# Kernel optimization log

Hardware: AMD Instinct MI355X
Metric: run time of the kernel (lower is better)

Reference implementation:

```python
import jax, jax.numpy as jnp
import numpy as np

D_MODEL = 1024
N_EXPERTS = 8
HIDDEN = 2048
TOP_K = 2


def setup_inputs() -> dict:
    key = jax.random.key(0)
    ks = jax.random.split(key, 5)
    scale_in = 1.0 / np.sqrt(D_MODEL)
    scale_h = 1.0 / np.sqrt(HIDDEN)
    return {
        "x": jax.random.normal(ks[0], (2, 2048, D_MODEL), dtype=jnp.float32),
        "w_router": jax.random.normal(ks[1], (D_MODEL, N_EXPERTS), dtype=jnp.float32) * scale_in,
        "w1": jax.random.normal(ks[2], (N_EXPERTS, D_MODEL, HIDDEN), dtype=jnp.float32) * scale_in,
        "w3": jax.random.normal(ks[3], (N_EXPERTS, D_MODEL, HIDDEN), dtype=jnp.float32) * scale_in,
        "w2": jax.random.normal(ks[4], (N_EXPERTS, HIDDEN, D_MODEL), dtype=jnp.float32) * scale_h,
    }


def reference(x, w_router, w1, w3, w2):
    orig_shape = x.shape
    xt = x.reshape(-1, orig_shape[-1])            # [T, D]
    T = xt.shape[0]

    # Router: linear -> softmax -> top-k (weights = top-k softmax scores)
    logits = xt @ w_router                         # [T, E]
    scores = jax.nn.softmax(logits, axis=-1)       # [T, E]
    top_w, top_idx = jax.lax.top_k(scores, TOP_K)  # [T, K]

    # Dense routing-weight matrix (reference form of dispatch/combine)
    dense_w = jnp.zeros((T, N_EXPERTS), dtype=scores.dtype)
    dense_w = dense_w.at[jnp.arange(T)[:, None], top_idx].set(top_w)  # [T, E]

    # Per-expert SwiGLU MLP over all tokens (dense reference of grouped GEMM)
    h1 = jnp.einsum('td,edh->teh', xt, w1)         # [T, E, H]
    h3 = jnp.einsum('td,edh->teh', xt, w3)
    h = jax.nn.silu(h1) * h3                       # [T, E, H]
    y = jnp.einsum('teh,ehd->ted', h, w2)          # [T, E, D]

    # Combine with routing weights
    out = jnp.einsum('te,ted->td', dense_w, y)     # [T, D]
    return out.reshape(orig_shape)
```

## Files before the change

kernel.cpp:

```cpp
#include <hip/hip_runtime.h>
#include <stdint.h>

#define D_MODEL 1024
#define N_EXP   8
#define HIDDEN  2048
#define TOPK    2

#define BK    32
#define PADM  128
#define NT1   (D_MODEL / BK)
#define NT2   (HIDDEN / BK)
#define G1X   1152
#define G2X   288

typedef short bf16x8 __attribute__((ext_vector_type(8)));
typedef float f32x4 __attribute__((ext_vector_type(4)));
typedef unsigned u32x4 __attribute__((ext_vector_type(4)));

__device__ __forceinline__ unsigned short f2bf(float f) {
    union { float f; unsigned u; } v; v.f = f;
    unsigned r = v.u + 0x7fffu + ((v.u >> 16) & 1u);
    return (unsigned short)(r >> 16);
}

__device__ __forceinline__ float bf2f(unsigned short u) {
    union { unsigned u; float f; } v; v.u = (unsigned)u << 16; return v.f;
}

__device__ __forceinline__ void gload_lds16(const void* g, void* l) {
    __builtin_amdgcn_global_load_lds(
        (const __attribute__((address_space(1))) void*)g,
        (__attribute__((address_space(3))) void*)l, 16, 0, 0);
}

__global__ __launch_bounds__(256) void k_prep(
    const float* __restrict__ x, const float* __restrict__ wr,
    const float* __restrict__ w1, const float* __restrict__ w3, const float* __restrict__ w2,
    unsigned short* __restrict__ xb,
    unsigned short* __restrict__ w13t, unsigned short* __restrict__ w2t,
    int* __restrict__ tok_e, float* __restrict__ tok_w,
    int* __restrict__ counts, int T, int nrouter)
{
    __shared__ unsigned tls[128][32];
    const int bx = blockIdx.x;
    const int tid = threadIdx.x;

    if (bx < nrouter) {
        int t = bx * 4 + (tid >> 6);
        int lane = tid & 63;
        if (t >= T) return;
        const float4* xr = (const float4*)(x + (size_t)t * D_MODEL);
        float acc[N_EXP];
#pragma unroll
        for (int e = 0; e < N_EXP; ++e) acc[e] = 0.f;
#pragma unroll
        for (int j = 0; j < 4; ++j) {
            int c = j * 64 + lane;
            float4 v = xr[c];
            ushort4 pk;
            pk.x = f2bf(v.x); pk.y = f2bf(v.y); pk.z = f2bf(v.z); pk.w = f2bf(v.w);
            *(ushort4*)(xb + (size_t)t * D_MODEL + c * 4) = pk;
            const float4* w4 = (const float4*)(wr + (size_t)c * 4 * N_EXP);
#pragma unroll
            for (int k = 0; k < 4; ++k) {
                float xv = (k == 0) ? v.x : (k == 1) ? v.y : (k == 2) ? v.z : v.w;
                float4 wa = w4[k * 2], wb = w4[k * 2 + 1];
                acc[0] += xv * wa.x; acc[1] += xv * wa.y; acc[2] += xv * wa.z; acc[3] += xv * wa.w;
                acc[4] += xv * wb.x; acc[5] += xv * wb.y; acc[6] += xv * wb.z; acc[7] += xv * wb.w;
            }
        }
#pragma unroll
        for (int off = 32; off > 0; off >>= 1) {
#pragma unroll
            for (int e = 0; e < N_EXP; ++e) acc[e] += __shfl_down(acc[e], off, 64);
        }
        if (lane == 0) {
            float mx = acc[0];
#pragma unroll
            for (int e = 1; e < N_EXP; ++e) mx = fmaxf(mx, acc[e]);
            float p[N_EXP], den = 0.f;
#pragma unroll
            for (int e = 0; e < N_EXP; ++e) { p[e] = __expf(acc[e] - mx); den += p[e]; }
            float inv = 1.f / den;
            int e0 = 0; float v0 = acc[0];
#pragma unroll
            for (int e = 1; e < N_EXP; ++e) if (acc[e] > v0) { v0 = acc[e]; e0 = e; }
            int e1 = -1; float v1 = -1e30f;
#pragma unroll
            for (int e = 0; e < N_EXP; ++e) if (e != e0 && acc[e] > v1) { v1 = acc[e]; e1 = e; }
            tok_e[2 * t] = e0;     tok_w[2 * t] = p[e0] * inv;
            tok_e[2 * t + 1] = e1; tok_w[2 * t + 1] = p[e1] * inv;
            atomicAdd(&counts[e0], 1);
            atomicAdd(&counts[e1], 1);
        }
        return;
    }

    const int b2 = bx - nrouter;
    const int z = b2 >> 8;
    const int inner = b2 & 255;
    const int mat = z >> 3, e = z & 7;
    const float* in; int Rr, Cc;
    if (mat == 0)      { in = w1; Rr = D_MODEL; Cc = HIDDEN; }
    else if (mat == 1) { in = w3; Rr = D_MODEL; Cc = HIDDEN; }
    else               { in = w2; Rr = HIDDEN; Cc = D_MODEL; }
    const size_t eb_in = (size_t)e * Rr * Cc;
    const int ntc = Cc >> 7;
    const int c0 = (inner % ntc) * 128;
    const int r0 = (inner / ntc) * 64;

    const int c4 = tid & 31;
    const int rbase = tid >> 5;
    float4 v[8];
#pragma unroll
    for (int p = 0; p < 8; ++p) {
        int row = p * 8 + rbase;
        v[p] = *(const float4*)(in + eb_in + (size_t)(r0 + row) * Cc + c0 + c4 * 4);
    }
    const unsigned swz = (unsigned)((c4 & 7) << 2);
#pragma unroll
    for (int p = 0; p < 8; ++p) {
        int row = p * 8 + rbase;
        unsigned x01 = (unsigned)f2bf(v[p].x) | ((unsigned)f2bf(v[p].y) << 16);
        unsigned x23 = (unsigned)f2bf(v[p].z) | ((unsigned)f2bf(v[p].w) << 16);
        unsigned p01 = __shfl_xor(x01, 32, 64);
        unsigned p23 = __shfl_xor(x23, 32, 64);
        int rr = row >> 1;
        unsigned col = (unsigned)rr ^ swz;
        if ((row & 1) == 0) {
            tls[c4 * 4 + 0][col] = (x01 & 0xffffu) | (p01 << 16);
            tls[c4 * 4 + 1][col] = (x01 >> 16) | (p01 & 0xffff0000u);
        } else {
            tls[c4 * 4 + 2][col] = (p23 & 0xffffu) | (x23 << 16);
            tls[c4 * 4 + 3][col] = (p23 >> 16) | (x23 & 0xffff0000u);
        }
    }
    __syncthreads();

    if (mat < 2) {
        const size_t eb = (size_t)e * (2 * HIDDEN) * D_MODEL;
        const int moff = mat ? 16 : 0;
#pragma unroll
        for (int p = 0; p < 4; ++p) {
            int li = p * 256 + tid;
            int c = li >> 3;
            int j = li & 7;
            unsigned s2 = (unsigned)(((c >> 2) & 7) << 2);
            u32x4 d = *(const u32x4*)(&tls[c][(unsigned)(j * 4) ^ s2]);
            int C = c0 + c;
            int r13 = ((C >> 4) << 5) + moff + (C & 15);
            *(u32x4*)(&w13t[eb + (size_t)r13 * D_MODEL + r0 + j * 8]) = d;
        }
    } else {
        const size_t eb = (size_t)e * D_MODEL * HIDDEN;
#pragma unroll
        for (int p = 0; p < 4; ++p) {
            int li = p * 256 + tid;
            int c = li >> 3;
            int j = li & 7;
            unsigned s2 = (unsigned)(((c >> 2) & 7) << 2);
            u32x4 d = *(const u32x4*)(&tls[c][(unsigned)(j * 4) ^ s2]);
            *(u32x4*)(&w2t[eb + (size_t)(c0 + c) * HIDDEN + r0 + j * 8]) = d;
        }
    }
}

__global__ void k_scan_scatter(const int* __restrict__ counts,
                               const int* __restrict__ tok_e, const float* __restrict__ tok_w,
                               int* __restrict__ offs,
                               int* __restrict__ row_token, float* __restrict__ row_weight,
                               int* __restrict__ tok_pos, int T) {
    __shared__ int scurs[N_EXP];
    if (threadIdx.x == 0) {
        int s = 0;
        for (int e = 0; e < N_EXP; ++e) {
            offs[e] = s; scurs[e] = s;
            s += ((counts[e] + PADM - 1) / PADM) * PADM;
        }
        offs[N_EXP] = s;
    }
    __syncthreads();
    for (int i = threadIdx.x; i < 2 * T; i += blockDim.x) {
        int e = tok_e[i];
        int pos = atomicAdd(&scurs[e], 1);
        row_token[pos] = i >> 1;
        row_weight[pos] = tok_w[i];
        tok_pos[i] = pos;
    }
}

__global__ __launch_bounds__(256, 2) void k_gemm1(
    const unsigned short* __restrict__ xb,
    const unsigned short* __restrict__ w13t,
    const int* __restrict__ row_token,
    const float* __restrict__ row_weight,
    const int* __restrict__ offs,
    unsigned short* __restrict__ h)
{
    __shared__ unsigned short A[3][128 * BK];
    __shared__ unsigned short B[3][256 * BK];

    const int b = blockIdx.x;
    const int bs = (b & 7) * (G1X / 8) + (b >> 3);
    int e = 0, mt = 0, nt = 0, found = 0, at = 0;
#pragma unroll
    for (int ee = 0; ee < N_EXP; ++ee) {
        int me = (offs[ee + 1] - offs[ee]) >> 7;
        int te = me * 16;
        if (!found && bs < at + te) {
            int loc = bs - at;
            nt = loc / me;
            mt = loc - nt * me;
            e = ee; found = 1;
        }
        at += te;
    }
    if (!found) return;
    const int m0 = offs[e] + mt * 128;
    const int n0b = nt * 256;

    const int tid = threadIdx.x;
    const int lane = tid & 63, wn = tid >> 6;

    const unsigned short* asrc[2];
    unsigned aoff[2];
#pragma unroll
    for (int q = 0; q < 2; ++q) {
        int c = q * 256 + tid;
        int m = c >> 2, kc = c & 3;
        int kcs = kc ^ (m & 3);
        int tok = row_token[m0 + m];
        asrc[q] = xb + (size_t)tok * D_MODEL + kcs * 8;
        aoff[q] = (unsigned)c * 8u;
    }
    const unsigned short* bsrc[4];
    unsigned boff[4];
#pragma unroll
    for (int q = 0; q < 4; ++q) {
        int c = q * 256 + tid;
        int n = c >> 2, kc = c & 3;
        int kcs = kc ^ (n & 3);
        bsrc[q] = w13t + ((size_t)e * (2 * HIDDEN) + n0b + n) * D_MODEL + kcs * 8;
        boff[q] = (unsigned)c * 8u;
    }

    f32x4 acc[8][4];
    const f32x4 zf = {0.f, 0.f, 0.f, 0.f};
#pragma unroll
    for (int mi = 0; mi < 8; ++mi)
#pragma unroll
        for (int ni = 0; ni < 4; ++ni) acc[mi][ni] = zf;

#pragma unroll
    for (int t = 0; t < 2; ++t) {
        const int ko = t * BK;
        gload_lds16(asrc[0] + ko, &A[t][aoff[0]]);
        gload_lds16(asrc[1] + ko, &A[t][aoff[1]]);
        gload_lds16(bsrc[0] + ko, &B[t][boff[0]]);
        gload_lds16(bsrc[1] + ko, &B[t][boff[1]]);
        gload_lds16(bsrc[2] + ko, &B[t][boff[2]]);
        gload_lds16(bsrc[3] + ko, &B[t][boff[3]]);
    }

    int cur = 0;
#pragma unroll 1
    for (int kt = 0; kt < NT1; ++kt) {
        if (kt == NT1 - 1) asm volatile("s_waitcnt vmcnt(0)" ::: "memory");
        else               asm volatile("s_waitcnt vmcnt(6)" ::: "memory");
        __builtin_amdgcn_s_barrier();

        const unsigned short* Ac = &A[cur][0];
        const unsigned short* Bc = &B[cur][0];
        const int nb = (cur + 2 >= 3) ? (cur - 1) : (cur + 2);
        const int ko = (kt + 2) * BK;
        const bool pf = (kt + 2 < NT1);

        bf16x8 a[8], bf[4];
        const int ke = (lane >> 4) * 8;
#pragma unroll
        for (int mi = 0; mi < 8; ++mi) {
            int m = mi * 16 + (lane & 15);
            a[mi] = *(const bf16x8*)(&Ac[m * BK + (ke ^ ((m & 3) * 8))]);
        }
#pragma unroll
        for (int ni = 0; ni < 4; ++ni) {
            int n = wn * 64 + ni * 16 + (lane & 15);
            bf[ni] = *(const bf16x8*)(&Bc[n * BK + (ke ^ ((n & 3) * 8))]);
        }
        if (pf) {
            gload_lds16(asrc[0] + ko, &A[nb][aoff[0]]);
            gload_lds16(asrc[1] + ko, &A[nb][aoff[1]]);
            gload_lds16(bsrc[0] + ko, &B[nb][boff[0]]);
            gload_lds16(bsrc[1] + ko, &B[nb][boff[1]]);
            gload_lds16(bsrc[2] + ko, &B[nb][boff[2]]);
            gload_lds16(bsrc[3] + ko, &B[nb][boff[3]]);
        }
        __builtin_amdgcn_s_barrier();
        __builtin_amdgcn_s_setprio(1);
#pragma unroll
        for (int mi = 0; mi < 8; ++mi)
#pragma unroll
            for (int ni = 0; ni < 4; ++ni)
                acc[mi][ni] = __builtin_amdgcn_mfma_f32_16x16x32_bf16(a[mi], bf[ni], acc[mi][ni], 0, 0, 0);
        __builtin_amdgcn_s_setprio(0);
        cur = (cur == 2) ? 0 : (cur + 1);
    }

    const int g0 = (n0b + wn * 64) >> 5;
#pragma unroll
    for (int mi = 0; mi < 8; ++mi) {
#pragma unroll
        for (int r = 0; r < 4; ++r) {
            int m = mi * 16 + (lane >> 4) * 4 + r;
            float wgt = row_weight[m0 + m];
            size_t rowbase = (size_t)(m0 + m) * HIDDEN;
#pragma unroll
            for (int p = 0; p < 2; ++p) {
                float v1 = acc[mi][2 * p][r], v3 = acc[mi][2 * p + 1][r];
                float sv = v1 / (1.f + __expf(-v1));
                int hc = (g0 + p) * 16 + (lane & 15);
                h[rowbase + hc] = f2bf(sv * v3 * wgt);
            }
        }
    }
}

__global__ __launch_bounds__(256, 2) void k_gemm2(
    const unsigned short* __restrict__ hh,
    const unsigned short* __restrict__ w2t,
    const int* __restrict__ offs,
    unsigned short* __restrict__ y)
{
    __shared__ unsigned short A[3][128 * BK];
    __shared__ unsigned short B[3][256 * BK];

    const int b = blockIdx.x;
    const int bs = (b & 7) * (G2X / 8) + (b >> 3);
    int e = 0, mt = 0, nt = 0, found = 0, at = 0;
#pragma unroll
    for (int ee = 0; ee < N_EXP; ++ee) {
        int me = (offs[ee + 1] - offs[ee]) >> 7;
        int te = me * 4;
        if (!found && bs < at + te) {
            int loc = bs - at;
            nt = loc / me;
            mt = loc - nt * me;
            e = ee; found = 1;
        }
        at += te;
    }
    if (!found) return;
    const int m0 = offs[e] + mt * 128;
    const int n0 = nt * 256;

    const int tid = threadIdx.x;
    const int lane = tid & 63, wn = tid >> 6;

    const unsigned short* asrc[2];
    unsigned aoff[2];
#pragma unroll
    for (int q = 0; q < 2; ++q) {
        int c = q * 256 + tid;
        int m = c >> 2, kc = c & 3;
        int kcs = kc ^ (m & 3);
        asrc[q] = hh + (size_t)(m0 + m) * HIDDEN + kcs * 8;
        aoff[q] = (unsigned)c * 8u;
    }
    const unsigned short* bsrc[4];
    unsigned boff[4];
#pragma unroll
    for (int q = 0; q < 4; ++q) {
        int c = q * 256 + tid;
        int n = c >> 2, kc = c & 3;
        int kcs = kc ^ (n & 3);
        bsrc[q] = w2t + ((size_t)e * D_MODEL + n0 + n) * HIDDEN + kcs * 8;
        boff[q] = (unsigned)c * 8u;
    }

    f32x4 acc[8][4];
    const f32x4 zf = {0.f, 0.f, 0.f, 0.f};
#pragma unroll
    for (int mi = 0; mi < 8; ++mi)
#pragma unroll
        for (int ni = 0; ni < 4; ++ni) acc[mi][ni] = zf;

#pragma unroll
    for (int t = 0; t < 2; ++t) {
        const int ko = t * BK;
        gload_lds16(asrc[0] + ko, &A[t][aoff[0]]);
        gload_lds16(asrc[1] + ko, &A[t][aoff[1]]);
        gload_lds16(bsrc[0] + ko, &B[t][boff[0]]);
        gload_lds16(bsrc[1] + ko, &B[t][boff[1]]);
        gload_lds16(bsrc[2] + ko, &B[t][boff[2]]);
        gload_lds16(bsrc[3] + ko, &B[t][boff[3]]);
    }

    int cur = 0;
#pragma unroll 1
    for (int kt = 0; kt < NT2; ++kt) {
        if (kt == NT2 - 1) asm volatile("s_waitcnt vmcnt(0)" ::: "memory");
        else               asm volatile("s_waitcnt vmcnt(6)" ::: "memory");
        __builtin_amdgcn_s_barrier();

        const unsigned short* Ac = &A[cur][0];
        const unsigned short* Bc = &B[cur][0];
        const int nb = (cur + 2 >= 3) ? (cur - 1) : (cur + 2);
        const int ko = (kt + 2) * BK;
        const bool pf = (kt + 2 < NT2);

        bf16x8 a[8], bf[4];
        const int ke = (lane >> 4) * 8;
#pragma unroll
        for (int mi = 0; mi < 8; ++mi) {
            int m = mi * 16 + (lane & 15);
            a[mi] = *(const bf16x8*)(&Ac[m * BK + (ke ^ ((m & 3) * 8))]);
        }
#pragma unroll
        for (int ni = 0; ni < 4; ++ni) {
            int n = wn * 64 + ni * 16 + (lane & 15);
            bf[ni] = *(const bf16x8*)(&Bc[n * BK + (ke ^ ((n & 3) * 8))]);
        }
        if (pf) {
            gload_lds16(asrc[0] + ko, &A[nb][aoff[0]]);
            gload_lds16(asrc[1] + ko, &A[nb][aoff[1]]);
            gload_lds16(bsrc[0] + ko, &B[nb][boff[0]]);
            gload_lds16(bsrc[1] + ko, &B[nb][boff[1]]);
            gload_lds16(bsrc[2] + ko, &B[nb][boff[2]]);
            gload_lds16(bsrc[3] + ko, &B[nb][boff[3]]);
        }
        __builtin_amdgcn_s_barrier();
        __builtin_amdgcn_s_setprio(1);
#pragma unroll
        for (int mi = 0; mi < 8; ++mi)
#pragma unroll
            for (int ni = 0; ni < 4; ++ni)
                acc[mi][ni] = __builtin_amdgcn_mfma_f32_16x16x32_bf16(a[mi], bf[ni], acc[mi][ni], 0, 0, 0);
        __builtin_amdgcn_s_setprio(0);
        cur = (cur == 2) ? 0 : (cur + 1);
    }

#pragma unroll
    for (int mi = 0; mi < 8; ++mi) {
#pragma unroll
        for (int r = 0; r < 4; ++r) {
            int m = mi * 16 + (lane >> 4) * 4 + r;
            size_t rowbase = (size_t)(m0 + m) * D_MODEL + n0;
#pragma unroll
            for (int ni = 0; ni < 4; ++ni) {
                int n = wn * 64 + ni * 16 + (lane & 15);
                y[rowbase + n] = f2bf(acc[mi][ni][r]);
            }
        }
    }
}

__global__ void k_combine(const unsigned short* __restrict__ y,
                          const int* __restrict__ tok_pos,
                          float* __restrict__ out, int n8) {
    int i = blockIdx.x * blockDim.x + threadIdx.x;
    if (i >= n8) return;
    int t = i >> 7;
    int c = (i & 127) * 8;
    int p0 = tok_pos[2 * t];
    int p1 = tok_pos[2 * t + 1];
    bf16x8 v0 = *(const bf16x8*)(y + (size_t)p0 * D_MODEL + c);
    bf16x8 v1 = *(const bf16x8*)(y + (size_t)p1 * D_MODEL + c);
    float* op = out + (size_t)t * D_MODEL + c;
    float4 o0, o1;
    o0.x = bf2f((unsigned short)v0[0]) + bf2f((unsigned short)v1[0]);
    o0.y = bf2f((unsigned short)v0[1]) + bf2f((unsigned short)v1[1]);
    o0.z = bf2f((unsigned short)v0[2]) + bf2f((unsigned short)v1[2]);
    o0.w = bf2f((unsigned short)v0[3]) + bf2f((unsigned short)v1[3]);
    o1.x = bf2f((unsigned short)v0[4]) + bf2f((unsigned short)v1[4]);
    o1.y = bf2f((unsigned short)v0[5]) + bf2f((unsigned short)v1[5]);
    o1.z = bf2f((unsigned short)v0[6]) + bf2f((unsigned short)v1[6]);
    o1.w = bf2f((unsigned short)v0[7]) + bf2f((unsigned short)v1[7]);
    *(float4*)op = o0;
    *(float4*)(op + 4) = o1;
}

extern "C" void kernel_launch(void* const* d_in, const int* in_sizes, int n_in,
                              void* d_out, int out_size, void* d_ws, size_t ws_size,
                              hipStream_t stream) {
    const float* x  = (const float*)d_in[0];
    const float* wr = (const float*)d_in[1];
    const float* w1 = (const float*)d_in[2];
    const float* w3 = (const float*)d_in[3];
    const float* w2 = (const float*)d_in[4];
    float* out = (float*)d_out;

    const int T = in_sizes[0] / D_MODEL;
    const int Rp = T * TOPK + N_EXP * PADM;

    char* ws = (char*)d_ws;
    size_t o = 0;
    unsigned short* xb   = (unsigned short*)(ws + o); o += (size_t)T * D_MODEL * 2;
    unsigned short* h    = (unsigned short*)(ws + o); o += (size_t)Rp * HIDDEN * 2;
    unsigned short* w13t = (unsigned short*)(ws + o); o += (size_t)N_EXP * 2 * HIDDEN * D_MODEL * 2;
    unsigned short* w2t  = (unsigned short*)(ws + o); o += (size_t)N_EXP * D_MODEL * HIDDEN * 2;
    int*   row_token  = (int*)(ws + o);   o += (size_t)Rp * 4;
    float* row_weight = (float*)(ws + o); o += (size_t)Rp * 4;
    int*   tok_e      = (int*)(ws + o);   o += (size_t)2 * T * 4;
    float* tok_w      = (float*)(ws + o); o += (size_t)2 * T * 4;
    int*   tok_pos    = (int*)(ws + o);   o += (size_t)2 * T * 4;
    int*   counts     = (int*)(ws + o);   o += 16 * 4;
    int*   offs       = (int*)(ws + o);   o += 16 * 4;

    unsigned short* y = w13t;

    hipMemsetAsync(counts, 0, 16 * 4, stream);
    hipMemsetAsync(row_token, 0, (size_t)Rp * 4, stream);
    hipMemsetAsync(row_weight, 0, (size_t)Rp * 4, stream);

    const int nrouter = (T + 3) / 4;
    const int nprep = nrouter + 6144;
    k_prep<<<nprep, 256, 0, stream>>>(x, wr, w1, w3, w2, xb, w13t, w2t,
                                      tok_e, tok_w, counts, T, nrouter);

    k_scan_scatter<<<1, 1024, 0, stream>>>(counts, tok_e, tok_w, offs,
                                           row_token, row_weight, tok_pos, T);

    k_gemm1<<<G1X, 256, 0, stream>>>(xb, w13t, row_token, row_weight, offs, h);
    k_gemm2<<<G2X, 256, 0, stream>>>(h, w2t, offs, y);

    int n8 = T * D_MODEL / 8;
    k_combine<<<(n8 + 255) / 256, 256, 0, stream>>>(y, tok_pos, out, n8);
}
```

Measured before the change: 306.4 us.

## Move w2 conversion/transpose from prep kernel into extra gemm1 blocks

The w2 fp32-to-bf16 transpose work is moved out of the prep kernel and into 2048 extra blocks appended to the gemm1 grid, reusing gemm1's LDS as a staging tile. The idea is to overlap the memory-bound w2 conversion with the compute-bound gemm1 and to shorten the serial prep stage before the scan. The cost is a larger gemm1 grid whose extra blocks carry gemm1's LDS and launch-bounds footprint. Those blocks may also compete with the GEMM tiles for bandwidth and CU slots.

```diff
diff --git a/kernel.cpp b/kernel.cpp
--- a/kernel.cpp
+++ b/kernel.cpp
@@ -11,6 +11,8 @@
 #define NT1   (D_MODEL / BK)
 #define NT2   (HIDDEN / BK)
 #define G1X   1152
+#define G1W2  2048
+#define G1TOT (G1X + G1W2)
 #define G2X   288
 
 typedef short bf16x8 __attribute__((ext_vector_type(8)));
@@ -35,9 +37,9 @@
 
 __global__ __launch_bounds__(256) void k_prep(
     const float* __restrict__ x, const float* __restrict__ wr,
-    const float* __restrict__ w1, const float* __restrict__ w3, const float* __restrict__ w2,
+    const float* __restrict__ w1, const float* __restrict__ w3,
     unsigned short* __restrict__ xb,
-    unsigned short* __restrict__ w13t, unsigned short* __restrict__ w2t,
+    unsigned short* __restrict__ w13t,
     int* __restrict__ tok_e, float* __restrict__ tok_w,
     int* __restrict__ counts, int T, int nrouter)
 {
@@ -100,12 +102,10 @@
     const int z = b2 >> 8;
     const int inner = b2 & 255;
     const int mat = z >> 3, e = z & 7;
-    const float* in; int Rr, Cc;
-    if (mat == 0)      { in = w1; Rr = D_MODEL; Cc = HIDDEN; }
-    else if (mat == 1) { in = w3; Rr = D_MODEL; Cc = HIDDEN; }
-    else               { in = w2; Rr = HIDDEN; Cc = D_MODEL; }
-    const size_t eb_in = (size_t)e * Rr * Cc;
-    const int ntc = Cc >> 7;
+    const float* in = mat ? w3 : w1;
+    const int Cc = HIDDEN;
+    const size_t eb_in = (size_t)e * D_MODEL * HIDDEN;
+    const int ntc = HIDDEN >> 7;
     const int c0 = (inner % ntc) * 128;
     const int r0 = (inner / ntc) * 64;
 
@@ -137,31 +137,18 @@
     }
     __syncthreads();
 
-    if (mat < 2) {
-        const size_t eb = (size_t)e * (2 * HIDDEN) * D_MODEL;
-        const int moff = mat ? 16 : 0;
-#pragma unroll
-        for (int p = 0; p < 4; ++p) {
-            int li = p * 256 + tid;
-            int c = li >> 3;
-            int j = li & 7;
-            unsigned s2 = (unsigned)(((c >> 2) & 7) << 2);
-            u32x4 d = *(const u32x4*)(&tls[c][(unsigned)(j * 4) ^ s2]);
-            int C = c0 + c;
-            int r13 = ((C >> 4) << 5) + moff + (C & 15);
-            *(u32x4*)(&w13t[eb + (size_t)r13 * D_MODEL + r0 + j * 8]) = d;
-        }
-    } else {
-        const size_t eb = (size_t)e * D_MODEL * HIDDEN;
-#pragma unroll
-        for (int p = 0; p < 4; ++p) {
-            int li = p * 256 + tid;
-            int c = li >> 3;
-            int j = li & 7;
-            unsigned s2 = (unsigned)(((c >> 2) & 7) << 2);
-            u32x4 d = *(const u32x4*)(&tls[c][(unsigned)(j * 4) ^ s2]);
-            *(u32x4*)(&w2t[eb + (size_t)(c0 + c) * HIDDEN + r0 + j * 8]) = d;
-        }
+    const size_t eb = (size_t)e * (2 * HIDDEN) * D_MODEL;
+    const int moff = mat ? 16 : 0;
+#pragma unroll
+    for (int p = 0; p < 4; ++p) {
+        int li = p * 256 + tid;
+        int c = li >> 3;
+        int j = li & 7;
+        unsigned s2 = (unsigned)(((c >> 2) & 7) << 2);
+        u32x4 d = *(const u32x4*)(&tls[c][(unsigned)(j * 4) ^ s2]);
+        int C = c0 + c;
+        int r13 = ((C >> 4) << 5) + moff + (C & 15);
+        *(u32x4*)(&w13t[eb + (size_t)r13 * D_MODEL + r0 + j * 8]) = d;
     }
 }
 
@@ -192,6 +179,8 @@
 __global__ __launch_bounds__(256, 2) void k_gemm1(
     const unsigned short* __restrict__ xb,
     const unsigned short* __restrict__ w13t,
+    const float* __restrict__ w2,
+    unsigned short* __restrict__ w2t,
     const int* __restrict__ row_token,
     const float* __restrict__ row_weight,
     const int* __restrict__ offs,
@@ -200,7 +189,58 @@
     __shared__ unsigned short A[3][128 * BK];
     __shared__ unsigned short B[3][256 * BK];
 
-    const int b = blockIdx.x;
+    const int bxx = blockIdx.x;
+    const int tid = threadIdx.x;
+
+    if (bxx >= G1X) {
+        const int b2 = bxx - G1X;
+        const int e2 = b2 >> 8, inner = b2 & 255;
+        const size_t eb_in = (size_t)e2 * HIDDEN * D_MODEL;
+        const int c0 = (inner & 7) * 128;
+        const int r0 = (inner >> 3) * 64;
+        unsigned (*tls)[32] = (unsigned(*)[32])&A[0][0];
+
+        const int c4 = tid & 31;
+        const int rbase = tid >> 5;
+        float4 v[8];
+#pragma unroll
+        for (int p = 0; p < 8; ++p) {
+            int row = p * 8 + rbase;
+            v[p] = *(const float4*)(w2 + eb_in + (size_t)(r0 + row) * D_MODEL + c0 + c4 * 4);
+        }
+        const unsigned swz = (unsigned)((c4 & 7) << 2);
+#pragma unroll
+        for (int p = 0; p < 8; ++p) {
+            int row = p * 8 + rbase;
+            unsigned x01 = (unsigned)f2bf(v[p].x) | ((unsigned)f2bf(v[p].y) << 16);
+            unsigned x23 = (unsigned)f2bf(v[p].z) | ((unsigned)f2bf(v[p].w) << 16);
+            unsigned p01 = __shfl_xor(x01, 32, 64);
+            unsigned p23 = __shfl_xor(x23, 32, 64);
+            int rr = row >> 1;
+            unsigned col = (unsigned)rr ^ swz;
+            if ((row & 1) == 0) {
+                tls[c4 * 4 + 0][col] = (x01 & 0xffffu) | (p01 << 16);
+                tls[c4 * 4 + 1][col] = (x01 >> 16) | (p01 & 0xffff0000u);
+            } else {
+                tls[c4 * 4 + 2][col] = (p23 & 0xffffu) | (x23 << 16);
+                tls[c4 * 4 + 3][col] = (p23 >> 16) | (x23 & 0xffff0000u);
+            }
+        }
+        __syncthreads();
+        const size_t eb = (size_t)e2 * D_MODEL * HIDDEN;
+#pragma unroll
+        for (int p = 0; p < 4; ++p) {
+            int li = p * 256 + tid;
+            int c = li >> 3;
+            int j = li & 7;
+            unsigned s2 = (unsigned)(((c >> 2) & 7) << 2);
+            u32x4 d = *(const u32x4*)(&tls[c][(unsigned)(j * 4) ^ s2]);
+            *(u32x4*)(&w2t[eb + (size_t)(c0 + c) * HIDDEN + r0 + j * 8]) = d;
+        }
+        return;
+    }
+
+    const int b = bxx;
     const int bs = (b & 7) * (G1X / 8) + (b >> 3);
     int e = 0, mt = 0, nt = 0, found = 0, at = 0;
 #pragma unroll
@@ -219,7 +259,6 @@
     const int m0 = offs[e] + mt * 128;
     const int n0b = nt * 256;
 
-    const int tid = threadIdx.x;
     const int lane = tid & 63, wn = tid >> 6;
 
     const unsigned short* asrc[2];
@@ -513,14 +552,14 @@
     hipMemsetAsync(row_weight, 0, (size_t)Rp * 4, stream);
 
     const int nrouter = (T + 3) / 4;
-    const int nprep = nrouter + 6144;
-    k_prep<<<nprep, 256, 0, stream>>>(x, wr, w1, w3, w2, xb, w13t, w2t,
+    const int nprep = nrouter + 4096;
+    k_prep<<<nprep, 256, 0, stream>>>(x, wr, w1, w3, xb, w13t,
                                       tok_e, tok_w, counts, T, nrouter);
 
     k_scan_scatter<<<1, 1024, 0, stream>>>(counts, tok_e, tok_w, offs,
                                            row_token, row_weight, tok_pos, T);
 
-    k_gemm1<<<G1X, 256, 0, stream>>>(xb, w13t, row_token, row_weight, offs, h);
+    k_gemm1<<<G1TOT, 256, 0, stream>>>(xb, w13t, w2, w2t, row_token, row_weight, offs, h);
     k_gemm2<<<G2X, 256, 0, stream>>>(h, w2t, offs, y);
 
     int n8 = T * D_MODEL / 8;
```

After: 298.3 us. -2.7%, faster.
